# Kernel optimization log

Hardware: AMD Instinct MI355X
Metric: run time of the kernel (lower is better)

Reference implementation:

```python
import jax, jax.numpy as jnp
import numpy as np

A, H, C, N, M = 256, 1024, 1024, 8192, 4096


def _linear(x, W, b):
    return x @ W.T + b


def _cosine_similarity(key_vec, memory):
    # key_vec: (1, M), memory: (N, M)
    k = key_vec / (jnp.linalg.norm(key_vec, axis=1, keepdims=True) + 1e-16)
    m = memory / (jnp.linalg.norm(memory, axis=1, keepdims=True) + 1e-16)
    sim = m @ k.T  # (N, 1)
    # NOTE: faithful to torch: softmax over dim=1, which has size 1 -> all ones
    return jax.nn.softmax(sim, axis=1)


def _circular_convolution(w, s):
    # torch loops: result[i] = sum_j w[(i - j) % N, 0] * s[j, 0]
    # s is the (1, N) shift matrix, so s.shape[0] == 1 (faithful to the torch loop bounds)
    n = w.shape[0]
    J = s.shape[0]
    idx = (jnp.arange(n)[:, None] - jnp.arange(J)[None, :]) % n  # (n, J)
    return (w[idx, 0] @ s[:, 0])[:, None]  # (n, 1)


def _sharpen(w, gamma):
    w = w ** gamma
    return w / jnp.sum(w, axis=0, keepdims=True)


def _gru_step(x, h, W_ih, W_hh, b_ih, b_hh):
    # single-timestep PyTorch GRU cell math
    gi = x @ W_ih.T + b_ih
    gh = h @ W_hh.T + b_hh
    i_r, i_z, i_n = jnp.split(gi, 3, axis=1)
    h_r, h_z, h_n = jnp.split(gh, 3, axis=1)
    r = jax.nn.sigmoid(i_r + h_r)
    z = jax.nn.sigmoid(i_z + h_z)
    n = jnp.tanh(i_n + r * h_n)
    return (1.0 - z) * n + z * h


def setup_inputs() -> dict:
    key = jax.random.key(0)
    ks = jax.random.split(key, 16)
    s = 0.02
    f32 = jnp.float32
    return {
        'action': jax.random.normal(ks[0], (1, A), f32),
        'hidden_state': jax.random.normal(ks[1], (1, 1, H), f32),
        'prev_read_weight': jax.random.uniform(ks[2], (N, 1), f32) / N,
        'prev_write_weight': jax.random.uniform(ks[3], (N, 1), f32) / N,
        'prev_controller_hidden': jax.random.normal(ks[4], (1, 1, C), f32) * 0.1,
        'memory': jax.random.normal(ks[5], (N, M), f32),
        'W_ih': jax.random.normal(ks[6], (3 * C, A + H), f32) * s,
        'W_hh': jax.random.normal(ks[7], (3 * C, C), f32) * s,
        'b_ih': jnp.zeros((3 * C,), f32),
        'b_hh': jnp.zeros((3 * C,), f32),
        'W_read': jax.random.normal(ks[8], (M, C), f32) * s,
        'b_read': jnp.zeros((M,), f32),
        'W_write': jax.random.normal(ks[9], (M, C), f32) * s,
        'b_write': jnp.zeros((M,), f32),
        'W_add': jax.random.normal(ks[10], (M, C), f32) * s,
        'b_add': jnp.zeros((M,), f32),
        'W_erase': jax.random.normal(ks[11], (M, C), f32) * s,
        'b_erase': jnp.zeros((M,), f32),
        'W_shift': jax.random.normal(ks[12], (N, C), f32) * s,
        'b_shift': jnp.zeros((N,), f32),
        'W_gamma': jax.random.normal(ks[13], (1, C), f32) * s,
        'b_gamma': jnp.zeros((1,), f32),
        'W_gate': jax.random.normal(ks[14], (1, C), f32) * s,
        'b_gate': jnp.zeros((1,), f32),
    }


def reference(action, hidden_state, prev_read_weight, prev_write_weight,
              prev_controller_hidden, memory,
              W_ih, W_hh, b_ih, b_hh,
              W_read, b_read, W_write, b_write,
              W_add, b_add, W_erase, b_erase,
              W_shift, b_shift, W_gamma, b_gamma, W_gate, b_gate):
    x = jnp.concatenate([action.reshape(1, -1), hidden_state[-1]], axis=1)  # (1, A+H)
    h = _gru_step(x, prev_controller_hidden[0], W_ih, W_hh, b_ih, b_hh)     # (1, C)
    controller_out = h
    new_controller_hidden = h[None]  # (1, 1, C)

    read_key = _linear(controller_out, W_read, b_read)    # (1, M)
    write_key = _linear(controller_out, W_write, b_write)  # (1, M)
    read_weight = _cosine_similarity(read_key, memory)     # (N, 1)
    write_weight = _cosine_similarity(write_key, memory)   # (N, 1)

    g = jax.nn.sigmoid(_linear(controller_out, W_gate, b_gate))  # (1, 1)
    read_weight = g * read_weight + (1.0 - g) * prev_read_weight
    write_weight = g * write_weight + (1.0 - g) * prev_write_weight

    shift = jax.nn.softmax(_linear(controller_out, W_shift, b_shift), axis=1)  # (1, N)
    gamma = jax.nn.softplus(_linear(controller_out, W_gamma, b_gamma))         # (1, 1)

    read_weight = _sharpen(_circular_convolution(read_weight, shift), gamma)
    write_weight = _sharpen(_circular_convolution(write_weight, shift), gamma)

    read_vector = read_weight.T @ memory  # (1, M)
    add_vec = _linear(controller_out, W_add, b_add)      # (1, M)
    erase_vec = _linear(controller_out, W_erase, b_erase)  # (1, M)
    # memory write (computed but discarded, exactly as in the torch forward which
    # never stores the updated local `memory` back to self.memory)
    _ = memory * (1.0 - write_weight * erase_vec) + write_weight * add_vec

    return (read_vector, read_weight, write_weight, new_controller_hidden)
```

## Files before the change

kernel.cpp:

```cpp
#include <hip/hip_runtime.h>
#include <math.h>

#define AA 256
#define HH 1024
#define CC 1024
#define NN 8192
#define MM 4096

#define WS_G      0
#define WS_GAMMA  1
#define WS_SR     2
#define WS_SW     3
#define GI_OFF    4
#define GH_OFF    (GI_OFF + 3*CC)
#define TR_OFF    (GH_OFF + 3*CC)
#define TW_OFF    (TR_OFF + NN)
#define ACC_OFF   (TW_OFF + NN)

__device__ __forceinline__ float wave_reduce(float v) {
    #pragma unroll
    for (int o = 32; o > 0; o >>= 1) v += __shfl_down(v, o);
    return v;
}

__global__ __launch_bounds__(256) void k_gru_gates(
    const float* __restrict__ action, const float* __restrict__ hidden,
    const float* __restrict__ W_ih, const float* __restrict__ W_hh,
    const float* __restrict__ b_ih, const float* __restrict__ b_hh,
    const float* __restrict__ hprev, float* __restrict__ ws)
{
    const int row = blockIdx.x;
    const int t = threadIdx.x;

    if (row < 16) ws[ACC_OFF + row * 256 + t] = 0.0f;
    if (row == 16 && t < 2) ws[WS_SR + t] = 0.0f;

    const float4* __restrict__ Wih4 = (const float4*)W_ih + (size_t)row * 320;
    const float4* __restrict__ Whh4 = (const float4*)W_hh + (size_t)row * 256;
    const float4* __restrict__ act4 = (const float4*)action;
    const float4* __restrict__ hid4 = (const float4*)hidden;
    const float4* __restrict__ hp4  = (const float4*)hprev;

    float si, sh;
    {
        float4 w = Wih4[t];
        float4 x = (t < 64) ? act4[t] : hid4[t - 64];
        si = w.x * x.x + w.y * x.y + w.z * x.z + w.w * x.w;
        if (t < 64) {
            float4 w2 = Wih4[256 + t];
            float4 x2 = hid4[192 + t];
            si += w2.x * x2.x + w2.y * x2.y + w2.z * x2.z + w2.w * x2.w;
        }
    }
    {
        float4 w = Whh4[t];
        float4 x = hp4[t];
        sh = w.x * x.x + w.y * x.y + w.z * x.z + w.w * x.w;
    }
    si = wave_reduce(si);
    sh = wave_reduce(sh);
    __shared__ float red[8];
    const int wid = t >> 6;
    if ((t & 63) == 0) { red[wid] = si; red[4 + wid] = sh; }
    __syncthreads();
    if (t == 0) {
        ws[GI_OFF + row] = red[0] + red[1] + red[2] + red[3] + b_ih[row];
        ws[GH_OFF + row] = red[4] + red[5] + red[6] + red[7] + b_hh[row];
    }
}

__global__ __launch_bounds__(1024) void k_gru_combine(
    const float* __restrict__ hprev,
    const float* __restrict__ W_gate, const float* __restrict__ b_gate,
    const float* __restrict__ W_gamma, const float* __restrict__ b_gamma,
    float* __restrict__ ws, float* __restrict__ d_out)
{
    const int c = threadIdx.x;
    const float* gi = ws + GI_OFF;
    const float* gh = ws + GH_OFF;
    const float r = 1.0f / (1.0f + expf(-(gi[c] + gh[c])));
    const float z = 1.0f / (1.0f + expf(-(gi[CC + c] + gh[CC + c])));
    const float n = tanhf(gi[2 * CC + c] + r * gh[2 * CC + c]);
    const float h = (1.0f - z) * n + z * hprev[c];
    d_out[MM + 2 * NN + c] = h;

    float vg = h * W_gate[c];
    float vm = h * W_gamma[c];
    vg = wave_reduce(vg);
    vm = wave_reduce(vm);
    __shared__ float rg[16], rm[16];
    const int wid = c >> 6;
    if ((c & 63) == 0) { rg[wid] = vg; rm[wid] = vm; }
    __syncthreads();
    if (c == 0) {
        float sg = 0.0f, sm = 0.0f;
        #pragma unroll
        for (int i = 0; i < 16; ++i) { sg += rg[i]; sm += rm[i]; }
        sg += b_gate[0];
        sm += b_gamma[0];
        ws[WS_G] = 1.0f / (1.0f + expf(-sg));
        ws[WS_GAMMA] = (sm > 20.0f) ? sm : log1pf(expf(sm));
    }
}

__global__ __launch_bounds__(256) void k_weights(
    const float* __restrict__ prev_r, const float* __restrict__ prev_w,
    float* __restrict__ ws)
{
    const int i = blockIdx.x * 256 + threadIdx.x;
    const float g = ws[WS_G];
    const float gamma = ws[WS_GAMMA];
    float tr = powf(g + (1.0f - g) * prev_r[i], gamma);
    float tw = powf(g + (1.0f - g) * prev_w[i], gamma);
    ws[TR_OFF + i] = tr;
    ws[TW_OFF + i] = tw;
    tr = wave_reduce(tr);
    tw = wave_reduce(tw);
    __shared__ float rr[4], rw[4];
    const int wid = threadIdx.x >> 6;
    if ((threadIdx.x & 63) == 0) { rr[wid] = tr; rw[wid] = tw; }
    __syncthreads();
    if (threadIdx.x == 0) {
        atomicAdd(&ws[WS_SR], rr[0] + rr[1] + rr[2] + rr[3]);
        atomicAdd(&ws[WS_SW], rw[0] + rw[1] + rw[2] + rw[3]);
    }
}

__global__ __launch_bounds__(256) void k_readvec(
    const float* __restrict__ memory, float* __restrict__ ws)
{
    __shared__ float tch[32];
    const int t = threadIdx.x;
    const int row0 = blockIdx.y * 32;
    if (t < 32) tch[t] = ws[TR_OFF + row0 + t];
    __syncthreads();
    const int c4 = blockIdx.x * 256 + t;
    const float4* __restrict__ mem4 = (const float4*)memory;
    float ax = 0.0f, ay = 0.0f, az = 0.0f, aw = 0.0f;
    #pragma unroll 4
    for (int r = 0; r < 32; ++r) {
        float4 m = mem4[(size_t)(row0 + r) * 1024 + c4];
        const float w = tch[r];
        ax += w * m.x; ay += w * m.y; az += w * m.z; aw += w * m.w;
    }
    float* acc = ws + ACC_OFF;
    atomicAdd(&acc[c4 * 4 + 0], ax);
    atomicAdd(&acc[c4 * 4 + 1], ay);
    atomicAdd(&acc[c4 * 4 + 2], az);
    atomicAdd(&acc[c4 * 4 + 3], aw);
}

__global__ __launch_bounds__(256) void k_finalize(
    const float* __restrict__ ws, float* __restrict__ d_out)
{
    const int idx = blockIdx.x * 256 + threadIdx.x;
    const float Sr = ws[WS_SR];
    const float Sw = ws[WS_SW];
    if (idx < MM)            d_out[idx] = ws[ACC_OFF + idx] / Sr;
    else if (idx < MM + NN)  d_out[idx] = ws[TR_OFF + idx - MM] / Sr;
    else                     d_out[idx] = ws[TW_OFF + idx - MM - NN] / Sw;
}

extern "C" void kernel_launch(void* const* d_in, const int* in_sizes, int n_in,
                              void* d_out, int out_size, void* d_ws, size_t ws_size,
                              hipStream_t stream)
{
    const float* action = (const float*)d_in[0];
    const float* hidden = (const float*)d_in[1];
    const float* prev_r = (const float*)d_in[2];
    const float* prev_w = (const float*)d_in[3];
    const float* hprev  = (const float*)d_in[4];
    const float* memory = (const float*)d_in[5];
    const float* W_ih   = (const float*)d_in[6];
    const float* W_hh   = (const float*)d_in[7];
    const float* b_ih   = (const float*)d_in[8];
    const float* b_hh   = (const float*)d_in[9];
    const float* W_gamma = (const float*)d_in[20];
    const float* b_gamma = (const float*)d_in[21];
    const float* W_gate  = (const float*)d_in[22];
    const float* b_gate  = (const float*)d_in[23];

    float* ws  = (float*)d_ws;
    float* out = (float*)d_out;

    hipLaunchKernelGGL(k_gru_gates, dim3(3 * CC), dim3(256), 0, stream,
                       action, hidden, W_ih, W_hh, b_ih, b_hh, hprev, ws);
    hipLaunchKernelGGL(k_gru_combine, dim3(1), dim3(1024), 0, stream,
                       hprev, W_gate, b_gate, W_gamma, b_gamma, ws, out);
    hipLaunchKernelGGL(k_weights, dim3(NN / 256), dim3(256), 0, stream,
                       prev_r, prev_w, ws);
    hipLaunchKernelGGL(k_readvec, dim3(4, 256), dim3(256), 0, stream,
                       memory, ws);
    hipLaunchKernelGGL(k_finalize, dim3((MM + 2 * NN) / 256), dim3(256), 0, stream,
                       ws, out);
}
```

Baseline: 329.6 us.

## Fuse weight computation into read-vector kernel and replace atomics with partial-sum reduction

```diff
diff --git a/kernel.cpp b/kernel.cpp
--- a/kernel.cpp
+++ b/kernel.cpp
@@ -15,7 +15,7 @@
 #define GH_OFF    (GI_OFF + 3*CC)
 #define TR_OFF    (GH_OFF + 3*CC)
 #define TW_OFF    (TR_OFF + NN)
-#define ACC_OFF   (TW_OFF + NN)
+#define P_OFF     (TW_OFF + NN)
 
 __device__ __forceinline__ float wave_reduce(float v) {
     #pragma unroll
@@ -29,11 +29,9 @@
     const float* __restrict__ b_ih, const float* __restrict__ b_hh,
     const float* __restrict__ hprev, float* __restrict__ ws)
 {
-    const int row = blockIdx.x;
     const int t = threadIdx.x;
-
-    if (row < 16) ws[ACC_OFF + row * 256 + t] = 0.0f;
-    if (row == 16 && t < 2) ws[WS_SR + t] = 0.0f;
+    const int wid = t >> 6, lane = t & 63;
+    const int row = blockIdx.x * 4 + wid;
 
     const float4* __restrict__ Wih4 = (const float4*)W_ih + (size_t)row * 320;
     const float4* __restrict__ Whh4 = (const float4*)W_hh + (size_t)row * 256;
@@ -41,31 +39,30 @@
     const float4* __restrict__ hid4 = (const float4*)hidden;
     const float4* __restrict__ hp4  = (const float4*)hprev;
 
-    float si, sh;
-    {
-        float4 w = Wih4[t];
-        float4 x = (t < 64) ? act4[t] : hid4[t - 64];
-        si = w.x * x.x + w.y * x.y + w.z * x.z + w.w * x.w;
-        if (t < 64) {
-            float4 w2 = Wih4[256 + t];
-            float4 x2 = hid4[192 + t];
-            si += w2.x * x2.x + w2.y * x2.y + w2.z * x2.z + w2.w * x2.w;
-        }
-    }
-    {
-        float4 w = Whh4[t];
-        float4 x = hp4[t];
-        sh = w.x * x.x + w.y * x.y + w.z * x.z + w.w * x.w;
-    }
+    float4 a[5], b[4], xa[5], xb[4];
+    #pragma unroll
+    for (int j = 0; j < 5; ++j) a[j] = Wih4[lane + 64 * j];
+    #pragma unroll
+    for (int j = 0; j < 4; ++j) b[j] = Whh4[lane + 64 * j];
+    xa[0] = act4[lane];
+    #pragma unroll
+    for (int j = 1; j < 5; ++j) xa[j] = hid4[lane + 64 * (j - 1)];
+    #pragma unroll
+    for (int j = 0; j < 4; ++j) xb[j] = hp4[lane + 64 * j];
+
+    float si = 0.0f, sh = 0.0f;
+    #pragma unroll
+    for (int j = 0; j < 5; ++j)
+        si += a[j].x * xa[j].x + a[j].y * xa[j].y + a[j].z * xa[j].z + a[j].w * xa[j].w;
+    #pragma unroll
+    for (int j = 0; j < 4; ++j)
+        sh += b[j].x * xb[j].x + b[j].y * xb[j].y + b[j].z * xb[j].z + b[j].w * xb[j].w;
+
     si = wave_reduce(si);
     sh = wave_reduce(sh);
-    __shared__ float red[8];
-    const int wid = t >> 6;
-    if ((t & 63) == 0) { red[wid] = si; red[4 + wid] = sh; }
-    __syncthreads();
-    if (t == 0) {
-        ws[GI_OFF + row] = red[0] + red[1] + red[2] + red[3] + b_ih[row];
-        ws[GH_OFF + row] = red[4] + red[5] + red[6] + red[7] + b_hh[row];
+    if (lane == 0) {
+        ws[GI_OFF + row] = si + b_ih[row];
+        ws[GH_OFF + row] = sh + b_hh[row];
     }
 }
 
@@ -76,6 +73,8 @@
     float* __restrict__ ws, float* __restrict__ d_out)
 {
     const int c = threadIdx.x;
+    if (c == 1) ws[WS_SR] = 0.0f;
+    if (c == 2) ws[WS_SW] = 0.0f;
     const float* gi = ws + GI_OFF;
     const float* gh = ws + GH_OFF;
     const float r = 1.0f / (1.0f + expf(-(gi[c] + gh[c])));
@@ -103,62 +102,77 @@
     }
 }
 
-__global__ __launch_bounds__(256) void k_weights(
+__global__ __launch_bounds__(256) void k_readvec(
+    const float* __restrict__ memory,
     const float* __restrict__ prev_r, const float* __restrict__ prev_w,
     float* __restrict__ ws)
 {
-    const int i = blockIdx.x * 256 + threadIdx.x;
-    const float g = ws[WS_G];
-    const float gamma = ws[WS_GAMMA];
-    float tr = powf(g + (1.0f - g) * prev_r[i], gamma);
-    float tw = powf(g + (1.0f - g) * prev_w[i], gamma);
-    ws[TR_OFF + i] = tr;
-    ws[TW_OFF + i] = tw;
-    tr = wave_reduce(tr);
-    tw = wave_reduce(tw);
-    __shared__ float rr[4], rw[4];
-    const int wid = threadIdx.x >> 6;
-    if ((threadIdx.x & 63) == 0) { rr[wid] = tr; rw[wid] = tw; }
-    __syncthreads();
-    if (threadIdx.x == 0) {
-        atomicAdd(&ws[WS_SR], rr[0] + rr[1] + rr[2] + rr[3]);
-        atomicAdd(&ws[WS_SW], rw[0] + rw[1] + rw[2] + rw[3]);
-    }
-}
-
-__global__ __launch_bounds__(256) void k_readvec(
-    const float* __restrict__ memory, float* __restrict__ ws)
-{
     __shared__ float tch[32];
     const int t = threadIdx.x;
-    const int row0 = blockIdx.y * 32;
-    if (t < 32) tch[t] = ws[TR_OFF + row0 + t];
+    const int bx = blockIdx.x;
+    const int by = blockIdx.y;
+    const int row0 = by * 32;
+
+    if (t < 32) {
+        const float g = ws[WS_G];
+        const float gamma = ws[WS_GAMMA];
+        const float tr = powf(g + (1.0f - g) * prev_r[row0 + t], gamma);
+        tch[t] = tr;
+        if (bx == 0) {
+            const float tw = powf(g + (1.0f - g) * prev_w[row0 + t], gamma);
+            ws[TR_OFF + row0 + t] = tr;
+            ws[TW_OFF + row0 + t] = tw;
+            float sr = tr, sw = tw;
+            #pragma unroll
+            for (int o = 16; o > 0; o >>= 1) {
+                sr += __shfl_down(sr, o);
+                sw += __shfl_down(sw, o);
+            }
+            if (t == 0) { atomicAdd(&ws[WS_SR], sr); atomicAdd(&ws[WS_SW], sw); }
+        }
+    }
     __syncthreads();
-    const int c4 = blockIdx.x * 256 + t;
-    const float4* __restrict__ mem4 = (const float4*)memory;
+
+    const int c4 = bx * 256 + t;
+    const float4* __restrict__ mem4 = (const float4*)memory + (size_t)row0 * 1024 + c4;
     float ax = 0.0f, ay = 0.0f, az = 0.0f, aw = 0.0f;
-    #pragma unroll 4
-    for (int r = 0; r < 32; ++r) {
-        float4 m = mem4[(size_t)(row0 + r) * 1024 + c4];
-        const float w = tch[r];
-        ax += w * m.x; ay += w * m.y; az += w * m.z; aw += w * m.w;
-    }
-    float* acc = ws + ACC_OFF;
-    atomicAdd(&acc[c4 * 4 + 0], ax);
-    atomicAdd(&acc[c4 * 4 + 1], ay);
-    atomicAdd(&acc[c4 * 4 + 2], az);
-    atomicAdd(&acc[c4 * 4 + 3], aw);
+    #pragma unroll
+    for (int grp = 0; grp < 4; ++grp) {
+        float4 m[8];
+        #pragma unroll
+        for (int j = 0; j < 8; ++j)
+            m[j] = mem4[(size_t)(grp * 8 + j) * 1024];
+        #pragma unroll
+        for (int j = 0; j < 8; ++j) {
+            const float w = tch[grp * 8 + j];
+            ax += w * m[j].x; ay += w * m[j].y; az += w * m[j].z; aw += w * m[j].w;
+        }
+    }
+    float4 acc; acc.x = ax; acc.y = ay; acc.z = az; acc.w = aw;
+    ((float4*)(ws + P_OFF))[(size_t)by * 1024 + c4] = acc;
 }
 
 __global__ __launch_bounds__(256) void k_finalize(
     const float* __restrict__ ws, float* __restrict__ d_out)
 {
-    const int idx = blockIdx.x * 256 + threadIdx.x;
-    const float Sr = ws[WS_SR];
-    const float Sw = ws[WS_SW];
-    if (idx < MM)            d_out[idx] = ws[ACC_OFF + idx] / Sr;
-    else if (idx < MM + NN)  d_out[idx] = ws[TR_OFF + idx - MM] / Sr;
-    else                     d_out[idx] = ws[TW_OFF + idx - MM - NN] / Sw;
+    const int t = threadIdx.x, b = blockIdx.x;
+    if (b < 16) {
+        const int col = b * 256 + t;
+        const float* __restrict__ P = ws + P_OFF;
+        float s0 = 0.0f, s1 = 0.0f, s2 = 0.0f, s3 = 0.0f;
+        #pragma unroll 8
+        for (int yb = 0; yb < 256; yb += 4) {
+            s0 += P[(size_t)(yb + 0) * 4096 + col];
+            s1 += P[(size_t)(yb + 1) * 4096 + col];
+            s2 += P[(size_t)(yb + 2) * 4096 + col];
+            s3 += P[(size_t)(yb + 3) * 4096 + col];
+        }
+        d_out[col] = (s0 + s1 + s2 + s3) / ws[WS_SR];
+    } else {
+        const int idx = (b - 16) * 256 + t;
+        d_out[MM + idx] = (idx < NN) ? ws[TR_OFF + idx] / ws[WS_SR]
+                                     : ws[TW_OFF + idx - NN] / ws[WS_SW];
+    }
 }
 
 extern "C" void kernel_launch(void* const* d_in, const int* in_sizes, int n_in,
@@ -183,14 +197,12 @@
     float* ws  = (float*)d_ws;
     float* out = (float*)d_out;
 
-    hipLaunchKernelGGL(k_gru_gates, dim3(3 * CC), dim3(256), 0, stream,
+    hipLaunchKernelGGL(k_gru_gates, dim3(3 * CC / 4), dim3(256), 0, stream,
                        action, hidden, W_ih, W_hh, b_ih, b_hh, hprev, ws);
     hipLaunchKernelGGL(k_gru_combine, dim3(1), dim3(1024), 0, stream,
                        hprev, W_gate, b_gate, W_gamma, b_gamma, ws, out);
-    hipLaunchKernelGGL(k_weights, dim3(NN / 256), dim3(256), 0, stream,
-                       prev_r, prev_w, ws);
     hipLaunchKernelGGL(k_readvec, dim3(4, 256), dim3(256), 0, stream,
-                       memory, ws);
-    hipLaunchKernelGGL(k_finalize, dim3((MM + 2 * NN) / 256), dim3(256), 0, stream,
+                       memory, prev_r, prev_w, ws);
+    hipLaunchKernelGGL(k_finalize, dim3(80), dim3(256), 0, stream,
                        ws, out);
 }
```

Result: faster. 317.8 us (-3.6%).
